# Performance work log

Measured on AMD Instinct MI355X. Metric: run time of the kernel, lower is better.

## Reference

```python
import jax, jax.numpy as jnp
import numpy as np

TP, M, K, N_GLOBAL = 8, 4096, 8192, 8192
K_LOCAL = K // TP      # 1024
N_LOCAL = N_GLOBAL // TP  # 1024


def setup_inputs() -> dict:
    key = jax.random.key(0)
    k1, k2, k3 = jax.random.split(key, 3)
    # all_act[r] is rank r's local activation shard (M, K_local);
    # the fused kernel all-gathers these into the gathered buffer.
    all_act = jax.random.normal(k1, (TP, M, K_LOCAL), dtype=jnp.float32)
    # local_W: this rank's weight shard, full K rows, N_local columns.
    local_W = jax.random.normal(k2, (K, N_LOCAL), dtype=jnp.float32) / np.sqrt(K)
    bias = jax.random.normal(k3, (N_LOCAL,), dtype=jnp.float32)
    return {"all_act": all_act, "local_W": local_W, "bias": bias}


def reference(all_act, local_W, bias):
    # Kernel accumulates, per source rank r:
    #   acc += A_shard[r] (M, K_local) @ W[r*K_local:(r+1)*K_local] (K_local, N_local)
    # which equals A_full @ W_local with A_full the K-concat of shards.
    W_shards = local_W.reshape(TP, K_LOCAL, N_LOCAL)
    out = jnp.einsum('rmk,rkn->mn', all_act, W_shards)  # (M, N_local)
    return out + bias[None, :]
```

## Files before the change

### kernel.cpp

```cpp
#include <hip/hip_runtime.h>
#include <stdint.h>

#define TP_      8
#define M_DIM    4096
#define K_DIM    8192
#define N_DIM    1024
#define KL_      1024
#define BM       128
#define BN       128
#define BK       64
#define SPLITK   4
#define KSLICE   (K_DIM / SPLITK)
#define MN4      (M_DIM * N_DIM / 4)
#define KCHUNKS  (K_DIM / 32)

typedef _Float16 f16;
typedef f16 f16x8 __attribute__((ext_vector_type(8)));
typedef float f32x4 __attribute__((ext_vector_type(4)));

__device__ __forceinline__ f16x8 cvt8(float4 a, float4 b) {
    f16x8 r;
    r[0] = (f16)a.x; r[1] = (f16)a.y; r[2] = (f16)a.z; r[3] = (f16)a.w;
    r[4] = (f16)b.x; r[5] = (f16)b.y; r[6] = (f16)b.z; r[7] = (f16)b.w;
    return r;
}

__device__ __forceinline__ void lds_load16(const void* g, void* l) {
    __builtin_amdgcn_global_load_lds(
        (const __attribute__((address_space(1))) void*)g,
        (__attribute__((address_space(3))) void*)l, 16, 0, 0);
}


__global__ __launch_bounds__(256) void conv_a_kernel(
        const float* __restrict__ act, f16* __restrict__ Afrag) {
    const int t = threadIdx.x;
    const int chunkId = blockIdx.x * 4 + (t >> 6);
    const int lane = t & 63;
    const int q  = lane >> 4;
    const int rr = lane & 15;
    const int mg  = chunkId >> 8;
    const int k32 = chunkId & 255;
    const int k  = k32 * 32 + q * 8;
    const int r  = k >> 10;
    const int kl = k & (KL_ - 1);
    const int m  = mg * 16 + rr;
    const float4* src = (const float4*)(act + ((size_t)r * M_DIM + m) * KL_ + kl);
    float4 a = src[0], b = src[1];
    *(f16x8*)(Afrag + (size_t)chunkId * 512 + lane * 8) = cvt8(a, b);
}

__global__ __launch_bounds__(256) void conv_w_kernel(
        const float* __restrict__ W, f16* __restrict__ Bfrag) {
    __shared__ float tile[64][68];
    const int t  = threadIdx.x;
    const int n0 = blockIdx.x * 64;
    const int k0 = blockIdx.y * 64;
    #pragma unroll
    for (int l = 0; l < 4; l++) {
        int kr = l * 16 + (t >> 4);
        float4 v = *(const float4*)&W[(size_t)(k0 + kr) * N_DIM + n0 + (t & 15) * 4];
        *(float4*)&tile[kr][(t & 15) * 4] = v;
    }
    __syncthreads();
    const int jtl   = t >> 6;
    const int kt32l = (t >> 5) & 1;
    const int u     = t & 31;
    const int rr    = u & 15;
    const int qp    = u >> 4;
    f16x8 h0, h1;
    #pragma unroll
    for (int kk = 0; kk < 8; kk++)
        h0[kk] = (f16)tile[kt32l * 32 + qp * 16 + kk][jtl * 16 + rr];
    #pragma unroll
    for (int kk = 0; kk < 8; kk++)
        h1[kk] = (f16)tile[kt32l * 32 + qp * 16 + 8 + kk][jtl * 16 + rr];
    size_t chunk = (size_t)(n0 / 16 + jtl) * KCHUNKS + (k0 / 32 + kt32l);
    f16* dst = Bfrag + chunk * 512;
    *(f16x8*)(dst + ((2 * qp)     * 16 + rr) * 8) = h0;
    *(f16x8*)(dst + ((2 * qp + 1) * 16 + rr) * 8) = h1;
}

__global__ __launch_bounds__(256, 4) void gemm_fused_kernel(
        const f16* __restrict__ Afrag,
        const f16* __restrict__ Bfrag,
        float* __restrict__ part) {
    __shared__ f16 sA[16 * 512];
    __shared__ f16 sB[16 * 512];

    const int tid  = threadIdx.x;
    const int w    = tid >> 6;
    const int lane = tid & 63;
    const int q    = lane >> 4;
    const int rr   = lane & 15;

    const int id   = blockIdx.x;
    const int xcd  = id & 7;
    const int z    = xcd >> 1;
    const int half = xcd & 1;
    const int slot = id >> 3;
    const int nb   = half * 4 + (slot & 3);
    const int mb   = slot >> 2;
    const int row0 = mb * BM;
    const int col0 = nb * BN;
    const int kb   = z * KSLICE;

    f32x4 acc[2][8];
    #pragma unroll
    for (int i = 0; i < 2; i++)
        #pragma unroll
        for (int j = 0; j < 8; j++)
            acc[i][j] = (f32x4){0.f, 0.f, 0.f, 0.f};

    const int NIT = KSLICE / BK;
    for (int it = 0; it < NIT; ++it) {
        const int kt32 = (kb + it * BK) >> 5;
        __syncthreads();
        #pragma unroll
        for (int c = 0; c < 4; c++) {
            int ci  = w * 4 + c;
            int kk2 = ci >> 3;
            int wi  = ci & 7;
            const f16* g = Afrag + ((size_t)((row0 >> 4) + wi) * KCHUNKS + kt32 + kk2) * 512 + lane * 8;
            lds_load16(g, &sA[ci * 512 + lane * 8]);
        }
        #pragma unroll
        for (int c = 0; c < 4; c++) {
            int ci  = w * 4 + c;
            int kk2 = ci >> 3;
            int j   = ci & 7;
            const f16* g = Bfrag + ((size_t)((col0 >> 4) + j) * KCHUNKS + kt32 + kk2) * 512 + lane * 8;
            lds_load16(g, &sB[ci * 512 + lane * 8]);
        }
        __syncthreads();

        #pragma unroll
        for (int s = 0; s < 2; s++) {
            f16x8 a0 = *(const f16x8*)&sA[(s * 8 + w * 2)     * 512 + lane * 8];
            f16x8 a1 = *(const f16x8*)&sA[(s * 8 + w * 2 + 1) * 512 + lane * 8];
            #pragma unroll
            for (int j = 0; j < 8; j++) {
                f16x8 bh = *(const f16x8*)&sB[(s * 8 + j) * 512 + lane * 8];
                acc[0][j] = __builtin_amdgcn_mfma_f32_16x16x32_f16(a0, bh, acc[0][j], 0, 0, 0);
                acc[1][j] = __builtin_amdgcn_mfma_f32_16x16x32_f16(a1, bh, acc[1][j], 0, 0, 0);
            }
        }
    }

    float* Pz = part + (size_t)z * M_DIM * N_DIM;
    #pragma unroll
    for (int i = 0; i < 2; i++)
        #pragma unroll
        for (int j = 0; j < 8; j++) {
            int gm = row0 + w * 32 + i * 16 + q * 4;
            int gn = col0 + j * 16 + rr;
            #pragma unroll
            for (int r2 = 0; r2 < 4; r2++)
                Pz[(size_t)(gm + r2) * N_DIM + gn] = acc[i][j][r2];
        }
}

__global__ __launch_bounds__(256) void reduce_kernel(
        const float* __restrict__ part, const float* __restrict__ bias,
        float* __restrict__ out) {
    int p = blockIdx.x * 256 + threadIdx.x;
    const float4* P = (const float4*)part;
    float4 s0 = P[p];
    float4 s1 = P[p + MN4];
    float4 s2 = P[p + 2 * MN4];
    float4 s3 = P[p + 3 * MN4];
    float4 b  = ((const float4*)bias)[p & (N_DIM / 4 - 1)];
    float4 r;
    r.x = s0.x + s1.x + s2.x + s3.x + b.x;
    r.y = s0.y + s1.y + s2.y + s3.y + b.y;
    r.z = s0.z + s1.z + s2.z + s3.z + b.z;
    r.w = s0.w + s1.w + s2.w + s3.w + b.w;
    ((float4*)out)[p] = r;
}

__global__ void gemm_fallback_kernel(const float* __restrict__ act,
                                     const float* __restrict__ W,
                                     const float* __restrict__ bias,
                                     float* __restrict__ out) {
    __shared__ float sA2[32][33];
    __shared__ float sB2[32][33];
    int tx = threadIdx.x, ty = threadIdx.y;
    int m = blockIdx.y * 32 + ty;
    int n = blockIdx.x * 32 + tx;
    float acc = 0.f;
    for (int kt = 0; kt < K_DIM; kt += 32) {
        int ka = kt + tx;
        int r = ka >> 10, kl = ka & (KL_ - 1);
        sA2[ty][tx] = act[((size_t)r * M_DIM + m) * KL_ + kl];
        sB2[ty][tx] = W[(size_t)(kt + ty) * N_DIM + n];
        __syncthreads();
        #pragma unroll
        for (int kk = 0; kk < 32; kk++) acc += sA2[ty][kk] * sB2[kk][tx];
        __syncthreads();
    }
    out[(size_t)m * N_DIM + n] = acc + bias[n];
}

extern "C" void kernel_launch(void* const* d_in, const int* in_sizes, int n_in,
                              void* d_out, int out_size, void* d_ws, size_t ws_size,
                              hipStream_t stream) {
    const float* all_act = (const float*)d_in[0];
    const float* local_W = (const float*)d_in[1];
    const float* bias    = (const float*)d_in[2];
    float* out = (float*)d_out;

    const size_t partBytes = (size_t)SPLITK * M_DIM * N_DIM * sizeof(float);
    const size_t elemsA    = (size_t)M_DIM * K_DIM;
    const size_t elemsW    = (size_t)K_DIM * N_DIM;
    const size_t need = partBytes + elemsA * sizeof(f16) + elemsW * sizeof(f16);

    if (ws_size < need) {
        gemm_fallback_kernel<<<dim3(N_DIM / 32, M_DIM / 32), dim3(32, 32), 0, stream>>>(
            all_act, local_W, bias, out);
        return;
    }

    float* part  = (float*)d_ws;
    f16*   Afrag = (f16*)((char*)d_ws + partBytes);
    f16*   Bfrag = Afrag + elemsA;

    conv_a_kernel<<<(M_DIM / 16) * (K_DIM / 32) / 4, 256, 0, stream>>>(all_act, Afrag);
    conv_w_kernel<<<dim3(N_DIM / 64, K_DIM / 64), 256, 0, stream>>>(local_W, Bfrag);
    gemm_fused_kernel<<<1024, 256, 0, stream>>>(Afrag, Bfrag, part);
    reduce_kernel<<<MN4 / 256, 256, 0, stream>>>(part, bias, out);
}
```

Baseline: 309.3 us.

## Fuse fp32-to-fp16 conversion into GEMM with register-prefetched double-buffered LDS

Removes the separate A and W conversion kernels and their fp16 workspace round trip. The GEMM now loads fp32 activations and weights directly into registers, converts them and writes MFMA-fragment layout into double-buffered LDS, prefetching the next K step while computing the current one. Tiles grow to 256x256 with 512 threads and BK=32, giving 256 blocks, and partial results use nontemporal stores. The cost is that each block re-reads fp32 inputs (twice the bytes of fp16), weight loads are strided scalar column reads, register pressure is higher, and the grid is smaller.

New measurement: 372.9 us. +20.6%, slower.

```diff
diff --git a/kernel.cpp b/kernel.cpp
--- a/kernel.cpp
+++ b/kernel.cpp
@@ -6,158 +6,152 @@
 #define K_DIM    8192
 #define N_DIM    1024
 #define KL_      1024
-#define BM       128
-#define BN       128
-#define BK       64
+#define BM       256
+#define BN       256
+#define BK       32
 #define SPLITK   4
 #define KSLICE   (K_DIM / SPLITK)
+#define NSTEP    (KSLICE / BK)
 #define MN4      (M_DIM * N_DIM / 4)
-#define KCHUNKS  (K_DIM / 32)
 
 typedef _Float16 f16;
 typedef f16 f16x8 __attribute__((ext_vector_type(8)));
 typedef float f32x4 __attribute__((ext_vector_type(4)));
 
-__device__ __forceinline__ f16x8 cvt8(float4 a, float4 b) {
-    f16x8 r;
-    r[0] = (f16)a.x; r[1] = (f16)a.y; r[2] = (f16)a.z; r[3] = (f16)a.w;
-    r[4] = (f16)b.x; r[5] = (f16)b.y; r[6] = (f16)b.z; r[7] = (f16)b.w;
-    return r;
-}
-
-__device__ __forceinline__ void lds_load16(const void* g, void* l) {
-    __builtin_amdgcn_global_load_lds(
-        (const __attribute__((address_space(1))) void*)g,
-        (__attribute__((address_space(3))) void*)l, 16, 0, 0);
-}
-
-
-__global__ __launch_bounds__(256) void conv_a_kernel(
-        const float* __restrict__ act, f16* __restrict__ Afrag) {
-    const int t = threadIdx.x;
-    const int chunkId = blockIdx.x * 4 + (t >> 6);
-    const int lane = t & 63;
-    const int q  = lane >> 4;
-    const int rr = lane & 15;
-    const int mg  = chunkId >> 8;
-    const int k32 = chunkId & 255;
-    const int k  = k32 * 32 + q * 8;
-    const int r  = k >> 10;
-    const int kl = k & (KL_ - 1);
-    const int m  = mg * 16 + rr;
-    const float4* src = (const float4*)(act + ((size_t)r * M_DIM + m) * KL_ + kl);
-    float4 a = src[0], b = src[1];
-    *(f16x8*)(Afrag + (size_t)chunkId * 512 + lane * 8) = cvt8(a, b);
-}
-
-__global__ __launch_bounds__(256) void conv_w_kernel(
-        const float* __restrict__ W, f16* __restrict__ Bfrag) {
-    __shared__ float tile[64][68];
-    const int t  = threadIdx.x;
-    const int n0 = blockIdx.x * 64;
-    const int k0 = blockIdx.y * 64;
-    #pragma unroll
-    for (int l = 0; l < 4; l++) {
-        int kr = l * 16 + (t >> 4);
-        float4 v = *(const float4*)&W[(size_t)(k0 + kr) * N_DIM + n0 + (t & 15) * 4];
-        *(float4*)&tile[kr][(t & 15) * 4] = v;
-    }
-    __syncthreads();
-    const int jtl   = t >> 6;
-    const int kt32l = (t >> 5) & 1;
-    const int u     = t & 31;
-    const int rr    = u & 15;
-    const int qp    = u >> 4;
-    f16x8 h0, h1;
-    #pragma unroll
-    for (int kk = 0; kk < 8; kk++)
-        h0[kk] = (f16)tile[kt32l * 32 + qp * 16 + kk][jtl * 16 + rr];
-    #pragma unroll
-    for (int kk = 0; kk < 8; kk++)
-        h1[kk] = (f16)tile[kt32l * 32 + qp * 16 + 8 + kk][jtl * 16 + rr];
-    size_t chunk = (size_t)(n0 / 16 + jtl) * KCHUNKS + (k0 / 32 + kt32l);
-    f16* dst = Bfrag + chunk * 512;
-    *(f16x8*)(dst + ((2 * qp)     * 16 + rr) * 8) = h0;
-    *(f16x8*)(dst + ((2 * qp + 1) * 16 + rr) * 8) = h1;
-}
-
-__global__ __launch_bounds__(256, 4) void gemm_fused_kernel(
-        const f16* __restrict__ Afrag,
-        const f16* __restrict__ Bfrag,
+#define BARRIER() do { \
+    asm volatile("s_waitcnt lgkmcnt(0)" ::: "memory"); \
+    __builtin_amdgcn_s_barrier(); \
+    asm volatile("" ::: "memory"); \
+} while (0)
+
+__global__ __launch_bounds__(512, 2) void gemm_fused_kernel(
+        const float* __restrict__ act,
+        const float* __restrict__ W,
         float* __restrict__ part) {
-    __shared__ f16 sA[16 * 512];
-    __shared__ f16 sB[16 * 512];
+    __shared__ f16 sm[2][32 * 512];
 
     const int tid  = threadIdx.x;
     const int w    = tid >> 6;
     const int lane = tid & 63;
     const int q    = lane >> 4;
     const int rr   = lane & 15;
+    const int wr   = w >> 2;
+    const int wc   = w & 3;
+
+    const int rt = tid >> 1;
+    const int hh = tid & 1;
 
     const int id   = blockIdx.x;
     const int xcd  = id & 7;
+    const int slot = id >> 3;
     const int z    = xcd >> 1;
-    const int half = xcd & 1;
-    const int slot = id >> 3;
-    const int nb   = half * 4 + (slot & 3);
-    const int mb   = slot >> 2;
+    const int mb   = (slot >> 2) * 2 + (xcd & 1);
+    const int nb   = slot & 3;
     const int row0 = mb * BM;
     const int col0 = nb * BN;
     const int kb   = z * KSLICE;
 
-    f32x4 acc[2][8];
+    float4 aa[4];
+    float  bb[16];
+
+    f32x4 acc[8][4];
     #pragma unroll
-    for (int i = 0; i < 2; i++)
+    for (int m = 0; m < 8; m++)
         #pragma unroll
-        for (int j = 0; j < 8; j++)
-            acc[i][j] = (f32x4){0.f, 0.f, 0.f, 0.f};
-
-    const int NIT = KSLICE / BK;
-    for (int it = 0; it < NIT; ++it) {
-        const int kt32 = (kb + it * BK) >> 5;
-        __syncthreads();
-        #pragma unroll
-        for (int c = 0; c < 4; c++) {
-            int ci  = w * 4 + c;
-            int kk2 = ci >> 3;
-            int wi  = ci & 7;
-            const f16* g = Afrag + ((size_t)((row0 >> 4) + wi) * KCHUNKS + kt32 + kk2) * 512 + lane * 8;
-            lds_load16(g, &sA[ci * 512 + lane * 8]);
-        }
-        #pragma unroll
-        for (int c = 0; c < 4; c++) {
-            int ci  = w * 4 + c;
-            int kk2 = ci >> 3;
-            int j   = ci & 7;
-            const f16* g = Bfrag + ((size_t)((col0 >> 4) + j) * KCHUNKS + kt32 + kk2) * 512 + lane * 8;
-            lds_load16(g, &sB[ci * 512 + lane * 8]);
-        }
-        __syncthreads();
-
-        #pragma unroll
-        for (int s = 0; s < 2; s++) {
-            f16x8 a0 = *(const f16x8*)&sA[(s * 8 + w * 2)     * 512 + lane * 8];
-            f16x8 a1 = *(const f16x8*)&sA[(s * 8 + w * 2 + 1) * 512 + lane * 8];
-            #pragma unroll
-            for (int j = 0; j < 8; j++) {
-                f16x8 bh = *(const f16x8*)&sB[(s * 8 + j) * 512 + lane * 8];
-                acc[0][j] = __builtin_amdgcn_mfma_f32_16x16x32_f16(a0, bh, acc[0][j], 0, 0, 0);
-                acc[1][j] = __builtin_amdgcn_mfma_f32_16x16x32_f16(a1, bh, acc[1][j], 0, 0, 0);
-            }
-        }
-    }
+        for (int n = 0; n < 4; n++)
+            acc[m][n] = (f32x4){0.f, 0.f, 0.f, 0.f};
+
+    const size_t aRowBase = (size_t)(row0 + rt) * KL_ + hh * 16;
+    const float* wColBase = W + col0 + rt;
+
+#define LOADT(step) do { \
+    const int kk_ = kb + (step) * BK; \
+    const int r_  = kk_ >> 10; \
+    const int kl_ = kk_ & (KL_ - 1); \
+    const float* ap = act + (size_t)r_ * ((size_t)M_DIM * KL_) + aRowBase + kl_; \
+    _Pragma("unroll") \
+    for (int i = 0; i < 4; i++) aa[i] = ((const float4*)ap)[i]; \
+    const float* wp = wColBase + (size_t)(kk_ + hh * 16) * N_DIM; \
+    _Pragma("unroll") \
+    for (int j = 0; j < 16; j++) bb[j] = wp[(size_t)j * N_DIM]; \
+} while (0)
+
+#define CVTWRITE(buf) do { \
+    f16x8 u0, u1, v0, v1; \
+    u0[0]=(f16)aa[0].x; u0[1]=(f16)aa[0].y; u0[2]=(f16)aa[0].z; u0[3]=(f16)aa[0].w; \
+    u0[4]=(f16)aa[1].x; u0[5]=(f16)aa[1].y; u0[6]=(f16)aa[1].z; u0[7]=(f16)aa[1].w; \
+    u1[0]=(f16)aa[2].x; u1[1]=(f16)aa[2].y; u1[2]=(f16)aa[2].z; u1[3]=(f16)aa[2].w; \
+    u1[4]=(f16)aa[3].x; u1[5]=(f16)aa[3].y; u1[6]=(f16)aa[3].z; u1[7]=(f16)aa[3].w; \
+    _Pragma("unroll") \
+    for (int j = 0; j < 8; j++) v0[j] = (f16)bb[j]; \
+    _Pragma("unroll") \
+    for (int j = 0; j < 8; j++) v1[j] = (f16)bb[8 + j]; \
+    f16* dA = &sm[buf][(rt >> 4) * 512]; \
+    *(f16x8*)(dA + ((2 * hh)     * 16 + (rt & 15)) * 8) = u0; \
+    *(f16x8*)(dA + ((2 * hh + 1) * 16 + (rt & 15)) * 8) = u1; \
+    f16* dB = &sm[buf][(16 + (rt >> 4)) * 512]; \
+    *(f16x8*)(dB + ((2 * hh)     * 16 + (rt & 15)) * 8) = v0; \
+    *(f16x8*)(dB + ((2 * hh + 1) * 16 + (rt & 15)) * 8) = v1; \
+} while (0)
+
+#define MFMAT(buf) do { \
+    const f16* base_ = sm[buf]; \
+    f16x8 bf[4]; \
+    _Pragma("unroll") \
+    for (int n = 0; n < 4; n++) \
+        bf[n] = *(const f16x8*)(base_ + (size_t)(16 + wc * 4 + n) * 512 + lane * 8); \
+    _Pragma("unroll") \
+    for (int mh = 0; mh < 2; mh++) { \
+        f16x8 af[4]; \
+        _Pragma("unroll") \
+        for (int mi = 0; mi < 4; mi++) \
+            af[mi] = *(const f16x8*)(base_ + (size_t)(wr * 8 + mh * 4 + mi) * 512 + lane * 8); \
+        _Pragma("unroll") \
+        for (int mi = 0; mi < 4; mi++) \
+            _Pragma("unroll") \
+            for (int n = 0; n < 4; n++) \
+                acc[mh * 4 + mi][n] = __builtin_amdgcn_mfma_f32_16x16x32_f16( \
+                    af[mi], bf[n], acc[mh * 4 + mi][n], 0, 0, 0); \
+    } \
+} while (0)
+
+    LOADT(0);
+    CVTWRITE(0);
+    LOADT(1);
+    BARRIER();
+
+    #pragma unroll 1
+    for (int t = 0; t < NSTEP - 2; t += 2) {
+        CVTWRITE(1);
+        LOADT(t + 2);
+        MFMAT(0);
+        BARRIER();
+        CVTWRITE(0);
+        LOADT(t + 3);
+        MFMAT(1);
+        BARRIER();
+    }
+    CVTWRITE(1);
+    MFMAT(0);
+    BARRIER();
+    MFMAT(1);
 
     float* Pz = part + (size_t)z * M_DIM * N_DIM;
     #pragma unroll
-    for (int i = 0; i < 2; i++)
+    for (int m = 0; m < 8; m++) {
+        const int gm = row0 + wr * 128 + m * 16 + q * 4;
         #pragma unroll
-        for (int j = 0; j < 8; j++) {
-            int gm = row0 + w * 32 + i * 16 + q * 4;
-            int gn = col0 + j * 16 + rr;
+        for (int n = 0; n < 4; n++) {
+            const int gn = col0 + wc * 64 + n * 16 + rr;
             #pragma unroll
             for (int r2 = 0; r2 < 4; r2++)
-                Pz[(size_t)(gm + r2) * N_DIM + gn] = acc[i][j][r2];
+                __builtin_nontemporal_store(acc[m][n][r2],
+                    &Pz[(size_t)(gm + r2) * N_DIM + gn]);
         }
+    }
+#undef LOADT
+#undef CVTWRITE
+#undef MFMAT
 }
 
 __global__ __launch_bounds__(256) void reduce_kernel(
@@ -210,22 +204,14 @@
     float* out = (float*)d_out;
 
     const size_t partBytes = (size_t)SPLITK * M_DIM * N_DIM * sizeof(float);
-    const size_t elemsA    = (size_t)M_DIM * K_DIM;
-    const size_t elemsW    = (size_t)K_DIM * N_DIM;
-    const size_t need = partBytes + elemsA * sizeof(f16) + elemsW * sizeof(f16);
-
-    if (ws_size < need) {
+
+    if (ws_size < partBytes) {
         gemm_fallback_kernel<<<dim3(N_DIM / 32, M_DIM / 32), dim3(32, 32), 0, stream>>>(
             all_act, local_W, bias, out);
         return;
     }
 
-    float* part  = (float*)d_ws;
-    f16*   Afrag = (f16*)((char*)d_ws + partBytes);
-    f16*   Bfrag = Afrag + elemsA;
-
-    conv_a_kernel<<<(M_DIM / 16) * (K_DIM / 32) / 4, 256, 0, stream>>>(all_act, Afrag);
-    conv_w_kernel<<<dim3(N_DIM / 64, K_DIM / 64), 256, 0, stream>>>(local_W, Bfrag);
-    gemm_fused_kernel<<<1024, 256, 0, stream>>>(Afrag, Bfrag, part);
+    float* part = (float*)d_ws;
+    gemm_fused_kernel<<<256, 512, 0, stream>>>(all_act, local_W, part);
     reduce_kernel<<<MN4 / 256, 256, 0, stream>>>(part, bias, out);
 }
```

## Rewrite GEMM as 256x256 tile, 8-wave double-buffered pipeline with interleaved staging

Applied to the files above, without the earlier changes.

Replaces the 128x128 tile GEMM with 256x256 tiles computed by 512-thread blocks (8 waves in a 2x4 grid). LDS is double-buffered, and the loads for the next K tile are interleaved with MFMA bursts, using explicit vmcnt waits, raw barriers, sched_barrier and setprio. The goal is to hide global-to-LDS latency and to raise arithmetic intensity per LDS byte. In exchange it uses far more registers (128 accumulator floats per thread), launches only 256 blocks, and depends on hand-tuned wait counts being correct.

After: 301.3 us. 1.03x faster.

```diff
diff --git a/kernel.cpp b/kernel.cpp
--- a/kernel.cpp
+++ b/kernel.cpp
@@ -6,11 +6,11 @@
 #define K_DIM    8192
 #define N_DIM    1024
 #define KL_      1024
-#define BM       128
-#define BN       128
-#define BK       64
+#define BM       256
+#define BN       256
 #define SPLITK   4
 #define KSLICE   (K_DIM / SPLITK)
+#define NT       (KSLICE / 64)
 #define MN4      (M_DIM * N_DIM / 4)
 #define KCHUNKS  (K_DIM / 32)
 
@@ -81,83 +81,146 @@
     *(f16x8*)(dst + ((2 * qp + 1) * 16 + rr) * 8) = h1;
 }
 
-__global__ __launch_bounds__(256, 4) void gemm_fused_kernel(
+__global__ __launch_bounds__(512, 2) void gemm_frag_kernel(
         const f16* __restrict__ Afrag,
         const f16* __restrict__ Bfrag,
         float* __restrict__ part) {
-    __shared__ f16 sA[16 * 512];
-    __shared__ f16 sB[16 * 512];
+    __shared__ f16 sm[2][64 * 512];
 
     const int tid  = threadIdx.x;
     const int w    = tid >> 6;
     const int lane = tid & 63;
     const int q    = lane >> 4;
     const int rr   = lane & 15;
+    const int wr   = w >> 2;
+    const int wc   = w & 3;
 
     const int id   = blockIdx.x;
     const int xcd  = id & 7;
+    const int slot = id >> 3;
     const int z    = xcd >> 1;
-    const int half = xcd & 1;
-    const int slot = id >> 3;
-    const int nb   = half * 4 + (slot & 3);
-    const int mb   = slot >> 2;
+    const int mb   = (slot >> 2) * 2 + (xcd & 1);
+    const int nb   = slot & 3;
     const int row0 = mb * BM;
     const int col0 = nb * BN;
-    const int kb   = z * KSLICE;
-
-    f32x4 acc[2][8];
-    #pragma unroll
-    for (int i = 0; i < 2; i++)
+    const int kb32 = z * (KSLICE / 32);
+    const int mg0  = row0 >> 4;
+    const int ng0  = col0 >> 4;
+
+    f32x4 acc[8][4];
+    #pragma unroll
+    for (int m = 0; m < 8; m++)
         #pragma unroll
-        for (int j = 0; j < 8; j++)
-            acc[i][j] = (f32x4){0.f, 0.f, 0.f, 0.f};
-
-    const int NIT = KSLICE / BK;
-    for (int it = 0; it < NIT; ++it) {
-        const int kt32 = (kb + it * BK) >> 5;
-        __syncthreads();
+        for (int n = 0; n < 4; n++)
+            acc[m][n] = (f32x4){0.f, 0.f, 0.f, 0.f};
+
+    f16x8 af[8];
+    f16x8 bf[2];
+
+#define STAGE_A(B_, T_, K2_) do { \
+    const int kt32_ = kb32 + 2 * (T_) + (K2_); \
+    _Pragma("unroll") \
+    for (int j_ = 0; j_ < 2; j_++) { \
+        const int mg_ = 2 * w + j_; \
+        const f16* g_ = Afrag + ((size_t)(mg0 + mg_) * KCHUNKS + kt32_) * 512 + lane * 8; \
+        lds_load16(g_, &sm[B_][(mg_ * 2 + (K2_)) * 512 + lane * 8]); \
+    } \
+} while (0)
+
+#define STAGE_B(B_, T_, K2_) do { \
+    const int kt32_ = kb32 + 2 * (T_) + (K2_); \
+    _Pragma("unroll") \
+    for (int j_ = 0; j_ < 2; j_++) { \
+        const int ng_ = 2 * w + j_; \
+        const f16* g_ = Bfrag + ((size_t)(ng0 + ng_) * KCHUNKS + kt32_) * 512 + lane * 8; \
+        lds_load16(g_, &sm[B_][(32 + ng_ * 2 + (K2_)) * 512 + lane * 8]); \
+    } \
+} while (0)
+
+#define READ_A(B_, K2_) do { \
+    _Pragma("unroll") \
+    for (int mi_ = 0; mi_ < 8; mi_++) \
+        af[mi_] = *(const f16x8*)&sm[B_][((wr * 8 + mi_) * 2 + (K2_)) * 512 + lane * 8]; \
+} while (0)
+
+#define READ_B(B_, K2_, NH_) do { \
+    _Pragma("unroll") \
+    for (int ni_ = 0; ni_ < 2; ni_++) \
+        bf[ni_] = *(const f16x8*)&sm[B_][(32 + (wc * 4 + (NH_) * 2 + ni_) * 2 + (K2_)) * 512 + lane * 8]; \
+} while (0)
+
+#define MFMA16(NH_) do { \
+    __builtin_amdgcn_s_setprio(1); \
+    _Pragma("unroll") \
+    for (int mi_ = 0; mi_ < 8; mi_++) \
+        _Pragma("unroll") \
+        for (int ni_ = 0; ni_ < 2; ni_++) \
+            acc[mi_][(NH_) * 2 + ni_] = __builtin_amdgcn_mfma_f32_16x16x32_f16( \
+                af[mi_], bf[ni_], acc[mi_][(NH_) * 2 + ni_], 0, 0, 0); \
+    __builtin_amdgcn_s_setprio(0); \
+} while (0)
+
+#define BAR() do { \
+    asm volatile("" ::: "memory"); \
+    __builtin_amdgcn_s_barrier(); \
+    asm volatile("" ::: "memory"); \
+} while (0)
+#define SBAR0() __builtin_amdgcn_sched_barrier(0)
+#define VM4() asm volatile("s_waitcnt vmcnt(4)" ::: "memory")
+#define VM0() asm volatile("s_waitcnt vmcnt(0)" ::: "memory")
+
+#define TILE(P_, T_, STG_, VMMID_, VMEND_) do { \
+    READ_A(P_, 0); READ_B(P_, 0, 0); \
+    if (STG_) STAGE_A((P_) ^ 1, (T_) + 1, 0); \
+    BAR(); SBAR0(); MFMA16(0); BAR(); \
+    READ_B(P_, 0, 1); \
+    if (STG_) STAGE_B((P_) ^ 1, (T_) + 1, 0); \
+    BAR(); SBAR0(); MFMA16(1); VMMID_; BAR(); \
+    READ_A(P_, 1); READ_B(P_, 1, 0); \
+    if (STG_) STAGE_A((P_) ^ 1, (T_) + 1, 1); \
+    BAR(); SBAR0(); MFMA16(0); BAR(); \
+    READ_B(P_, 1, 1); \
+    if (STG_) STAGE_B((P_) ^ 1, (T_) + 1, 1); \
+    BAR(); SBAR0(); MFMA16(1); VMEND_; BAR(); \
+} while (0)
+
+    STAGE_A(0, 0, 0);
+    STAGE_B(0, 0, 0);
+    STAGE_A(0, 0, 1);
+    STAGE_B(0, 0, 1);
+    VM4();
+    BAR();
+
+    #pragma unroll 1
+    for (int t = 0; t < 30; t += 2) {
+        TILE(0, t,     1, VM4(), VM4());
+        TILE(1, t + 1, 1, VM4(), VM4());
+    }
+    TILE(0, 30, 1, VM4(), VM4());
+    TILE(1, 31, 0, VM0(), (void)0);
+
+    float* Pz = part + (size_t)z * M_DIM * N_DIM;
+    #pragma unroll
+    for (int m = 0; m < 8; m++) {
+        const int gm = row0 + wr * 128 + m * 16 + q * 4;
         #pragma unroll
-        for (int c = 0; c < 4; c++) {
-            int ci  = w * 4 + c;
-            int kk2 = ci >> 3;
-            int wi  = ci & 7;
-            const f16* g = Afrag + ((size_t)((row0 >> 4) + wi) * KCHUNKS + kt32 + kk2) * 512 + lane * 8;
-            lds_load16(g, &sA[ci * 512 + lane * 8]);
-        }
-        #pragma unroll
-        for (int c = 0; c < 4; c++) {
-            int ci  = w * 4 + c;
-            int kk2 = ci >> 3;
-            int j   = ci & 7;
-            const f16* g = Bfrag + ((size_t)((col0 >> 4) + j) * KCHUNKS + kt32 + kk2) * 512 + lane * 8;
-            lds_load16(g, &sB[ci * 512 + lane * 8]);
-        }
-        __syncthreads();
-
-        #pragma unroll
-        for (int s = 0; s < 2; s++) {
-            f16x8 a0 = *(const f16x8*)&sA[(s * 8 + w * 2)     * 512 + lane * 8];
-            f16x8 a1 = *(const f16x8*)&sA[(s * 8 + w * 2 + 1) * 512 + lane * 8];
-            #pragma unroll
-            for (int j = 0; j < 8; j++) {
-                f16x8 bh = *(const f16x8*)&sB[(s * 8 + j) * 512 + lane * 8];
-                acc[0][j] = __builtin_amdgcn_mfma_f32_16x16x32_f16(a0, bh, acc[0][j], 0, 0, 0);
-                acc[1][j] = __builtin_amdgcn_mfma_f32_16x16x32_f16(a1, bh, acc[1][j], 0, 0, 0);
-            }
-        }
-    }
-
-    float* Pz = part + (size_t)z * M_DIM * N_DIM;
-    #pragma unroll
-    for (int i = 0; i < 2; i++)
-        #pragma unroll
-        for (int j = 0; j < 8; j++) {
-            int gm = row0 + w * 32 + i * 16 + q * 4;
-            int gn = col0 + j * 16 + rr;
+        for (int n = 0; n < 4; n++) {
+            const int gn = col0 + wc * 64 + n * 16 + rr;
             #pragma unroll
             for (int r2 = 0; r2 < 4; r2++)
-                Pz[(size_t)(gm + r2) * N_DIM + gn] = acc[i][j][r2];
+                Pz[(size_t)(gm + r2) * N_DIM + gn] = acc[m][n][r2];
         }
+    }
+#undef STAGE_A
+#undef STAGE_B
+#undef READ_A
+#undef READ_B
+#undef MFMA16
+#undef BAR
+#undef SBAR0
+#undef VM4
+#undef VM0
+#undef TILE
 }
 
 __global__ __launch_bounds__(256) void reduce_kernel(
@@ -226,6 +289,6 @@
 
     conv_a_kernel<<<(M_DIM / 16) * (K_DIM / 32) / 4, 256, 0, stream>>>(all_act, Afrag);
     conv_w_kernel<<<dim3(N_DIM / 64, K_DIM / 64), 256, 0, stream>>>(local_W, Bfrag);
-    gemm_fused_kernel<<<1024, 256, 0, stream>>>(Afrag, Bfrag, part);
+    gemm_frag_kernel<<<256, 512, 0, stream>>>(Afrag, Bfrag, part);
     reduce_kernel<<<MN4 / 256, 256, 0, stream>>>(part, bias, out);
 }
```
